# Kernel tuning notes

Measured on AMD Instinct MI355X. Metric: run time of the kernel, lower is better.

The kernel has to match this reference:

```python
import jax, jax.numpy as jnp
import numpy as np

N_NODES = {'movie': 50000, 'director': 10000, 'actor': 25000}
# relation name -> (src_type, dst_type, num_edges)
RELS = {'md': ('movie', 'director', 150000),
        'dm': ('director', 'movie', 150000),
        'ma': ('movie', 'actor', 300000),
        'am': ('actor', 'movie', 300000)}
F_IN, HID, HEADS, OUT = 1024, 256, 8, 4
HD = HID // HEADS  # 32 per-head dim


def setup_inputs() -> dict:
    key = jax.random.key(0)
    kit = iter(jax.random.split(key, 128))
    def nrm(shape, s):
        return jax.random.normal(next(kit), shape, jnp.float32) * s
    inp = {}
    for t, n in N_NODES.items():
        inp['x_' + t] = nrm((n, F_IN), 1.0)
    for rn, (st, dt, e) in RELS.items():
        inp['e_' + rn + '_src'] = jax.random.randint(next(kit), (e,), 0, N_NODES[st], dtype=jnp.int32)
        inp['e_' + rn + '_dst'] = jax.random.randint(next(kit), (e,), 0, N_NODES[dt], dtype=jnp.int32)
        inp['a_' + rn] = nrm((HEADS, HD, HD), 0.05)   # per-relation attention matrix
        inp['m_' + rn] = nrm((HEADS, HD, HD), 0.05)   # per-relation message matrix
        inp['p_' + rn] = jnp.ones((HEADS,), jnp.float32)  # relation priority
    for t in N_NODES:
        inp['W_in_' + t] = nrm((F_IN, HID), 0.02)
        inp['b_in_' + t] = jnp.zeros((HID,), jnp.float32)
        for nm in ('k', 'q', 'v'):
            inp['W' + nm + '_' + t] = nrm((HID, HID), 0.05)
            inp['b' + nm + '_' + t] = jnp.zeros((HID,), jnp.float32)
        inp['Wa_' + t] = nrm((HID, HID), 0.05)
        inp['ba_' + t] = jnp.zeros((HID,), jnp.float32)
        inp['skip_' + t] = jnp.array(1.0, jnp.float32)
    inp['W_out'] = nrm((HID, OUT), 0.05)
    inp['b_out'] = jnp.zeros((OUT,), jnp.float32)
    return inp


def _forward(p):
    # per-node-type input projection (the HGT.lin_dict step)
    h = {t: p['x_' + t] @ p['W_in_' + t] + p['b_in_' + t] for t in N_NODES}
    # per-type K/Q/V projections, reshaped to [N, H, D]
    def proj(nm):
        return {t: (h[t] @ p['W' + nm + '_' + t] + p['b' + nm + '_' + t]).reshape(-1, HEADS, HD)
                for t in N_NODES}
    k, q, v = proj('k'), proj('q'), proj('v')
    scale = 1.0 / np.sqrt(HD)
    # per-edge-type: gather, relation-transform, score
    buf = {t: [] for t in N_NODES}
    for rn, (st, dt, _) in RELS.items():
        si, di = p['e_' + rn + '_src'], p['e_' + rn + '_dst']
        ke = jnp.einsum('ehd,hdf->ehf', k[st][si], p['a_' + rn])  # [E,H,D]
        ve = jnp.einsum('ehd,hdf->ehf', v[st][si], p['m_' + rn])  # [E,H,D]
        al = (q[dt][di] * ke).sum(-1) * (p['p_' + rn] * scale)    # [E,H]
        buf[dt].append((di, al, ve))
    # destination-grouped segment softmax + scatter aggregation
    out = {}
    for t, n in N_NODES.items():
        di = jnp.concatenate([b[0] for b in buf[t]])
        al = jnp.concatenate([b[1] for b in buf[t]])
        ve = jnp.concatenate([b[2] for b in buf[t]])
        amax = jax.ops.segment_max(al, di, num_segments=n)        # [N,H]
        amax = jnp.where(jnp.isfinite(amax), amax, 0.0)
        ex = jnp.exp(al - amax[di])
        den = jax.ops.segment_sum(ex, di, num_segments=n)[di]
        w = ex / jnp.where(den > 0, den, 1.0)                     # [E,H]
        agg = jax.ops.segment_sum(w[:, :, None] * ve, di, num_segments=n).reshape(n, HID)
        o = jax.nn.gelu(agg @ p['Wa_' + t] + p['ba_' + t])
        beta = jax.nn.sigmoid(p['skip_' + t])                     # gated skip connection
        out[t] = beta * o + (1.0 - beta) * h[t]
    # final classifier on movie nodes
    return out['movie'] @ p['W_out'] + p['b_out']


def reference(x_movie, x_director, x_actor, e_md_src, e_md_dst, a_md, m_md, p_md, e_dm_src, e_dm_dst, a_dm, m_dm, p_dm, e_ma_src, e_ma_dst, a_ma, m_ma, p_ma, e_am_src, e_am_dst, a_am, m_am, p_am, W_in_movie, b_in_movie, Wk_movie, bk_movie, Wq_movie, bq_movie, Wv_movie, bv_movie, Wa_movie, ba_movie, skip_movie, W_in_director, b_in_director, Wk_director, bk_director, Wq_director, bq_director, Wv_director, bv_director, Wa_director, ba_director, skip_director, W_in_actor, b_in_actor, Wk_actor, bk_actor, Wq_actor, bq_actor, Wv_actor, bv_actor, Wa_actor, ba_actor, skip_actor, W_out, b_out):
    p = dict(locals())
    return _forward(p)
```

## Files before the change

kernel.cpp:

```cpp
#include <hip/hip_runtime.h>
#include <math.h>

#define NM 50000
#define ND 10000
#define NA 25000
#define E_DM 150000
#define E_AM 300000
#define E_TOT (E_DM + E_AM)
#define HID 256
#define HEADS 8
#define HD 32
#define FIN 1024
#define SCALE 0.17677669529663687f

typedef __attribute__((ext_vector_type(8))) short short8;
typedef __attribute__((ext_vector_type(4))) float f32x4;

typedef __attribute__((address_space(1))) const unsigned char gas_u8;
typedef __attribute__((address_space(3))) unsigned char las_u8;

__device__ __forceinline__ void gload16(const void* g, void* l) {
    gas_u8* gp = (gas_u8*)(unsigned long long)(uintptr_t)g;
    las_u8* lp = (las_u8*)(unsigned int)(uintptr_t)l;
    __builtin_amdgcn_global_load_lds((const __attribute__((address_space(1))) void*)gp,
                                     (__attribute__((address_space(3))) void*)lp, 16, 0, 0);
}

__device__ __forceinline__ unsigned int pk_bf16(float x, float y) {
    unsigned int a = __float_as_uint(x), b = __float_as_uint(y);
    a += 0x7FFFu + ((a >> 16) & 1u);
    b += 0x7FFFu + ((b >> 16) & 1u);
    return (a >> 16) | (b & 0xFFFF0000u);
}
__device__ __forceinline__ unsigned short to_bf16(float x) {
    unsigned int a = __float_as_uint(x);
    a += 0x7FFFu + ((a >> 16) & 1u);
    return (unsigned short)(a >> 16);
}
__device__ __forceinline__ float bf2f(unsigned short u) {
    return __uint_as_float(((unsigned int)u) << 16);
}

struct F4 { const float* W[4]; const float* b[4]; const float* a[4]; float* Wf[4]; float* bf[4]; };
__global__ void fold_w4(F4 f4) {
    int di = blockIdx.y;
    const float* W = f4.W[di]; const float* b = f4.b[di]; const float* a = f4.a[di];
    float* Wf = f4.Wf[di]; float* bf = f4.bf[di];
    int c = threadIdx.x;
    int h = c >> 5, f = c & 31;
    int r = blockIdx.x;
    float acc = 0.f;
    if (r < HID) {
        #pragma unroll
        for (int d = 0; d < HD; ++d)
            acc += W[r * HID + h * HD + d] * a[(h * HD + d) * HD + f];
        Wf[r * HID + c] = acc;
    } else {
        #pragma unroll
        for (int d = 0; d < HD; ++d)
            acc += b[h * HD + d] * a[(h * HD + d) * HD + f];
        bf[c] = acc;
    }
}

struct PDesc { const float* W; unsigned short* out; int K; int b0; };
struct PMulti { PDesc d[9]; int nd; };
__global__ void wt_pack(PMulti pm) {
    int bid = blockIdx.x; int di = 0;
    #pragma unroll
    for (int i = 1; i < 9; ++i) if (i < pm.nd && bid >= pm.d[i].b0) di = i;
    PDesc p = pm.d[di];
    int kstep = bid - p.b0;
    int t = threadIdx.x;
    #pragma unroll
    for (int i = 0; i < 32; ++i) {
        int idx = i * 256 + t;
        int n0 = idx >> 9, r = idx & 511, lane = r >> 3, j = r & 7;
        int k = kstep * 32 + (lane >> 4) * 8 + j;
        int c = n0 * 16 + (lane & 15);
        p.out[(size_t)kstep * 8192 + idx] = to_bf16(p.W[(size_t)k * HID + c]);
    }
}

struct GDesc {
    const void* A; const unsigned short* Bt; const float* bias; void* C;
    const void* hskip; const float* gate; int M; int K; int epi; int obf; int abf; int b0;
};
struct GMulti { GDesc d[5]; int nd; };

#define GBM 64

__launch_bounds__(512, 6)
__global__ void gemm_mfma(GMulti mu) {
    __shared__ unsigned short sB[2][16 * 512];
    __shared__ unsigned short sA[2][4 * 512];

    int bid = blockIdx.x;
    int di = 0;
    #pragma unroll
    for (int i = 1; i < 5; ++i)
        if (i < mu.nd && bid >= mu.d[i].b0) di = i;
    GDesc g = mu.d[di];
    int bm = (bid - g.b0) * GBM;
    int M = g.M, K = g.K;

    int t = threadIdx.x;
    int lane = t & 63;
    int w = t >> 6;
    int wp = w >> 1;
    int ch = w & 1;
    int l16 = lane & 15;

    int slot = t >> 1;
    int ss_ = slot >> 6;
    int sl  = slot & 63;
    int arow_f = bm + ss_ * 16 + (sl & 15);
    int ak0    = (sl >> 4) * 8 + (t & 1) * 4;
    const float* Ap = nullptr;
    const unsigned short* Abp = nullptr;
    if (g.abf) {
        if (w < 4) {
            int r = bm + w * 16 + l16;
            Abp = (const unsigned short*)g.A + (size_t)min(r, M - 1) * K + ((lane >> 4) * 8);
        }
    } else {
        Ap = (const float*)g.A + (size_t)min(arow_f, M - 1) * K + ak0;
    }

    f32x4 acc[8];
    #pragma unroll
    for (int n = 0; n < 8; ++n) acc[n] = (f32x4)(0.f);

    int nk = K >> 5;
    {
        const unsigned short* gB = g.Bt;
        gload16(gB + w * 512 + lane * 8, &sB[0][w * 512]);
        gload16(gB + (w + 8) * 512 + lane * 8, &sB[0][(w + 8) * 512]);
        if (g.abf) {
            if (w < 4) gload16(Abp, &sA[0][w * 512]);
        } else {
            float4 f = *(const float4*)(Ap);
            uint2 pk = make_uint2(pk_bf16(f.x, f.y), pk_bf16(f.z, f.w));
            *(uint2*)&sA[0][slot * 8 + (t & 1) * 4] = pk;
        }
    }
    __syncthreads();

    int cur = 0;
    for (int ks = 0; ks < nk; ++ks) {
        int nxt = cur ^ 1;
        bool pf = (ks + 1 < nk);
        float4 f;
        if (pf) {
            const unsigned short* gB = g.Bt + (size_t)(ks + 1) * 8192;
            gload16(gB + w * 512 + lane * 8, &sB[nxt][w * 512]);
            gload16(gB + (w + 8) * 512 + lane * 8, &sB[nxt][(w + 8) * 512]);
            if (g.abf) {
                if (w < 4) gload16(Abp + (ks + 1) * 32, &sA[nxt][w * 512]);
            } else {
                f = *(const float4*)(Ap + (ks + 1) * 32);
            }
        }
        short8 af = *(const short8*)&sA[cur][(wp * 64 + lane) * 8];
        short8 bfr[8];
        #pragma unroll
        for (int n = 0; n < 8; ++n)
            bfr[n] = *(const short8*)&sB[cur][((ch * 8 + n) * 64 + lane) * 8];
        #pragma unroll
        for (int n = 0; n < 8; ++n)
            acc[n] = __builtin_amdgcn_mfma_f32_16x16x32_bf16(af, bfr[n], acc[n], 0, 0, 0);
        if (pf && !g.abf) {
            uint2 pk = make_uint2(pk_bf16(f.x, f.y), pk_bf16(f.z, f.w));
            *(uint2*)&sA[nxt][slot * 8 + (t & 1) * 4] = pk;
        }
        __syncthreads();
        cur = nxt;
    }

    float beta = 0.f;
    if (g.epi) beta = 1.f / (1.f + expf(-g.gate[0]));
    int r0 = bm + wp * 16 + ((lane >> 4) << 2);
    #pragma unroll
    for (int n = 0; n < 8; ++n) {
        int col = ch * 128 + n * 16 + l16;
        #pragma unroll
        for (int j = 0; j < 4; ++j) {
            int grow = r0 + j;
            if (grow >= M) continue;
            float v = acc[n][j] + g.bias[col];
            if (g.epi) {
                float x = v;
                float gl = 0.5f * x * (1.f + tanhf(0.7978845608028654f * (x + 0.044715f * x * x * x)));
                float hv = bf2f(((const unsigned short*)g.hskip)[(size_t)grow * HID + col]);
                v = beta * gl + (1.f - beta) * hv;
            }
            if (g.obf) ((unsigned short*)g.C)[(size_t)grow * HID + col] = to_bf16(v);
            else ((float*)g.C)[(size_t)grow * HID + col] = v;
        }
    }
}

__global__ void hist_deg(const int* __restrict__ dA, const int* __restrict__ dB,
                         int* __restrict__ deg) {
    int i = blockIdx.x * 256 + threadIdx.x;
    if (i < E_DM) atomicAdd(&deg[dA[i]], 1);
    else if (i < E_TOT) atomicAdd(&deg[dB[i - E_DM]], 1);
}

__global__ void scan_pass1(const int* __restrict__ deg, int* __restrict__ bsum) {
    __shared__ int s[256];
    int b = blockIdx.x, t = threadIdx.x;
    int i = b * 256 + t;
    int v = (i < NM) ? deg[i] : 0;
    s[t] = v; __syncthreads();
    for (int off = 128; off > 0; off >>= 1) {
        if (t < off) s[t] += s[t + off];
        __syncthreads();
    }
    if (t == 0) bsum[b] = s[0];
}

__global__ void scan_pass2(const int* __restrict__ bsum, int* __restrict__ boff, int nb) {
    __shared__ int s[256];
    int t = threadIdx.x;
    int v = (t < nb) ? bsum[t] : 0;
    s[t] = v; __syncthreads();
    for (int off = 1; off < 256; off <<= 1) {
        int x = (t >= off) ? s[t - off] : 0;
        __syncthreads();
        s[t] += x;
        __syncthreads();
    }
    if (t < nb) boff[t] = s[t] - v;
}

__global__ void scan_pass3(const int* __restrict__ deg, const int* __restrict__ boff,
                           int* __restrict__ rowptr, int* __restrict__ cursor) {
    __shared__ int s[256];
    int b = blockIdx.x, t = threadIdx.x, i = b * 256 + t;
    int v = (i < NM) ? deg[i] : 0;
    s[t] = v; __syncthreads();
    for (int off = 1; off < 256; off <<= 1) {
        int x = (t >= off) ? s[t - off] : 0;
        __syncthreads();
        s[t] += x;
        __syncthreads();
    }
    int excl = s[t] - v + boff[b];
    if (i < NM) { rowptr[i] = excl; cursor[i] = excl; }
    if (i == 0) rowptr[NM] = E_TOT;
}

__global__ void fill_adj(const int* __restrict__ sA, const int* __restrict__ dA,
                         const int* __restrict__ sB, const int* __restrict__ dB,
                         int* __restrict__ cursor, int* __restrict__ adj) {
    int i = blockIdx.x * 256 + threadIdx.x;
    int d, entry;
    if (i < E_DM)      { d = dA[i];        entry = sA[i]; }
    else if (i < E_TOT){ int j = i - E_DM; d = dB[j]; entry = (sB[j] + ND) | (1 << 16); }
    else return;
    int pos = atomicAdd(&cursor[d], 1);
    adj[pos] = entry;
}

__launch_bounds__(256)
__global__ void agg_fused(const int* __restrict__ rowptr, const int* __restrict__ adj,
                          const unsigned short* __restrict__ q, const unsigned short* __restrict__ kt_all,
                          const unsigned short* __restrict__ vt_all,
                          const float* __restrict__ p_dm, const float* __restrict__ p_am,
                          unsigned short* __restrict__ agg) {
    int d = blockIdx.x * 4 + (threadIdx.x >> 6);
    if (d >= NM) return;
    int lane = threadIdx.x & 63;
    int h = lane >> 3;
    int start = rowptr[d], end = rowptr[d + 1];
    uint2 qu = *(const uint2*)(q + (size_t)d * HID + lane * 4);
    float q0 = __uint_as_float(qu.x << 16), q1 = __uint_as_float(qu.x & 0xFFFF0000u);
    float q2 = __uint_as_float(qu.y << 16), q3 = __uint_as_float(qu.y & 0xFFFF0000u);
    float pr0 = p_dm[h] * SCALE, pr1 = p_am[h] * SCALE;
    float m = -INFINITY, den = 0.f, a0 = 0.f, a1 = 0.f, a2 = 0.f, a3 = 0.f;
    for (int i = start; i < end; ++i) {
        int e = adj[i];
        int sr = e & 0xFFFF;
        uint2 ku = *(const uint2*)(kt_all + (size_t)sr * HID + lane * 4);
        float k0 = __uint_as_float(ku.x << 16), k1 = __uint_as_float(ku.x & 0xFFFF0000u);
        float k2 = __uint_as_float(ku.y << 16), k3 = __uint_as_float(ku.y & 0xFFFF0000u);
        float prod = q0 * k0 + q1 * k1 + q2 * k2 + q3 * k3;
        prod += __shfl_xor(prod, 1);
        prod += __shfl_xor(prod, 2);
        prod += __shfl_xor(prod, 4);
        float a = prod * ((e >> 16) ? pr1 : pr0);
        float mn = fmaxf(m, a);
        float c  = __expf(m - mn);
        float ex = __expf(a - mn);
        uint2 vu = *(const uint2*)(vt_all + (size_t)sr * HID + lane * 4);
        float v0 = __uint_as_float(vu.x << 16), v1 = __uint_as_float(vu.x & 0xFFFF0000u);
        float v2 = __uint_as_float(vu.y << 16), v3 = __uint_as_float(vu.y & 0xFFFF0000u);
        den = den * c + ex;
        a0 = a0 * c + ex * v0; a1 = a1 * c + ex * v1;
        a2 = a2 * c + ex * v2; a3 = a3 * c + ex * v3;
        m = mn;
    }
    float inv = (end > start) ? 1.f / den : 0.f;
    *(uint2*)(agg + (size_t)d * HID + lane * 4) =
        make_uint2(pk_bf16(a0 * inv, a1 * inv), pk_bf16(a2 * inv, a3 * inv));
}

__launch_bounds__(256)
__global__ void classifier(const float* __restrict__ X, const float* __restrict__ W,
                           const float* __restrict__ b, float* __restrict__ out, int M) {
    int t = threadIdx.x, lane = t & 63;
    int wid = blockIdx.x * 4 + (t >> 6);
    int nw = gridDim.x * 4;
    float w0[4], w1[4], w2[4], w3[4];
    #pragma unroll
    for (int j = 0; j < 4; ++j) {
        float4 wv = *(const float4*)(W + (lane * 4 + j) * 4);
        w0[j] = wv.x; w1[j] = wv.y; w2[j] = wv.z; w3[j] = wv.w;
    }
    float b0 = b[0], b1 = b[1], b2 = b[2], b3 = b[3];
    for (int row = wid; row < M; row += nw) {
        float4 x = *(const float4*)(X + (size_t)row * HID + lane * 4);
        float s0 = x.x * w0[0] + x.y * w0[1] + x.z * w0[2] + x.w * w0[3];
        float s1 = x.x * w1[0] + x.y * w1[1] + x.z * w1[2] + x.w * w1[3];
        float s2 = x.x * w2[0] + x.y * w2[1] + x.z * w2[2] + x.w * w2[3];
        float s3 = x.x * w3[0] + x.y * w3[1] + x.z * w3[2] + x.w * w3[3];
        #pragma unroll
        for (int off = 32; off > 0; off >>= 1) {
            s0 += __shfl_xor(s0, off); s1 += __shfl_xor(s1, off);
            s2 += __shfl_xor(s2, off); s3 += __shfl_xor(s3, off);
        }
        if (lane == 0) {
            float4 o = make_float4(s0 + b0, s1 + b1, s2 + b2, s3 + b3);
            *(float4*)(out + (size_t)row * 4) = o;
        }
    }
}

extern "C" void kernel_launch(void* const* d_in, const int* in_sizes, int n_in,
                              void* d_out, int out_size, void* d_ws, size_t ws_size,
                              hipStream_t stream) {
    (void)in_sizes; (void)n_in; (void)out_size; (void)ws_size;
    const float* x_movie    = (const float*)d_in[0];
    const float* x_director = (const float*)d_in[1];
    const float* x_actor    = (const float*)d_in[2];
    const int*   e_dm_src = (const int*)d_in[8];
    const int*   e_dm_dst = (const int*)d_in[9];
    const float* a_dm     = (const float*)d_in[10];
    const float* m_dm     = (const float*)d_in[11];
    const float* p_dm     = (const float*)d_in[12];
    const int*   e_am_src = (const int*)d_in[18];
    const int*   e_am_dst = (const int*)d_in[19];
    const float* a_am     = (const float*)d_in[20];
    const float* m_am     = (const float*)d_in[21];
    const float* p_am     = (const float*)d_in[22];
    const float* W_in_m = (const float*)d_in[23];
    const float* b_in_m = (const float*)d_in[24];
    const float* Wq_m   = (const float*)d_in[27];
    const float* bq_m   = (const float*)d_in[28];
    const float* Wa_m   = (const float*)d_in[31];
    const float* ba_m   = (const float*)d_in[32];
    const float* skip_m = (const float*)d_in[33];
    const float* W_in_d = (const float*)d_in[34];
    const float* b_in_d = (const float*)d_in[35];
    const float* Wk_d   = (const float*)d_in[36];
    const float* bk_d   = (const float*)d_in[37];
    const float* Wv_d   = (const float*)d_in[40];
    const float* bv_d   = (const float*)d_in[41];
    const float* W_in_a = (const float*)d_in[45];
    const float* b_in_a = (const float*)d_in[46];
    const float* Wk_a   = (const float*)d_in[47];
    const float* bk_a   = (const float*)d_in[48];
    const float* Wv_a   = (const float*)d_in[51];
    const float* bv_a   = (const float*)d_in[52];
    const float* W_out  = (const float*)d_in[56];
    const float* b_out  = (const float*)d_in[57];

    char* base = (char*)d_ws;
    size_t off = 0;
    auto alloc = [&](size_t bytes) -> void* {
        void* p = base + off;
        off = (off + bytes + 255) & ~(size_t)255;
        return p;
    };
    unsigned short* h_m = (unsigned short*)alloc((size_t)NM * HID * 2);
    unsigned short* h_d = (unsigned short*)alloc((size_t)ND * HID * 2);
    unsigned short* h_a = (unsigned short*)alloc((size_t)NA * HID * 2);
    unsigned short* q_m = (unsigned short*)alloc((size_t)NM * HID * 2);
    float* out_m  = (float*)alloc((size_t)NM * HID * 4);
    unsigned short* agg = (unsigned short*)alloc((size_t)NM * HID * 2);
    unsigned short* kt_all = (unsigned short*)alloc((size_t)(ND + NA) * HID * 2);
    unsigned short* vt_all = (unsigned short*)alloc((size_t)(ND + NA) * HID * 2);
    float* Wf     = (float*)alloc(4 * (size_t)HID * HID * 4);
    float* bf     = (float*)alloc(4 * (size_t)HID * 4);
    int* deg      = (int*)alloc(NM * 4);
    int* rowptr   = (int*)alloc((NM + 1) * 4);
    int* cursor   = (int*)alloc(NM * 4);
    int* bsum     = (int*)alloc(256 * 4);
    int* boff     = (int*)alloc(256 * 4);
    int* adj      = (int*)alloc((size_t)E_TOT * 4);
    unsigned short* Bt_in_m = (unsigned short*)alloc((size_t)256 * 1024 * 2);
    unsigned short* Bt_in_d = (unsigned short*)alloc((size_t)256 * 1024 * 2);
    unsigned short* Bt_in_a = (unsigned short*)alloc((size_t)256 * 1024 * 2);
    unsigned short* Bt_q_m  = (unsigned short*)alloc((size_t)256 * 256 * 2);
    unsigned short* Bt_k_dm = (unsigned short*)alloc((size_t)256 * 256 * 2);
    unsigned short* Bt_v_dm = (unsigned short*)alloc((size_t)256 * 256 * 2);
    unsigned short* Bt_k_am = (unsigned short*)alloc((size_t)256 * 256 * 2);
    unsigned short* Bt_v_am = (unsigned short*)alloc((size_t)256 * 256 * 2);
    unsigned short* Bt_a_m  = (unsigned short*)alloc((size_t)256 * 256 * 2);

    unsigned short* kt_dm = kt_all;
    unsigned short* kt_am = kt_all + (size_t)ND * HID;
    unsigned short* vt_dm = vt_all;
    unsigned short* vt_am = vt_all + (size_t)ND * HID;

    float* Wf_k_dm = Wf + 0 * HID * HID;  float* bf_k_dm = bf + 0 * HID;
    float* Wf_v_dm = Wf + 1 * HID * HID;  float* bf_v_dm = bf + 1 * HID;
    float* Wf_k_am = Wf + 2 * HID * HID;  float* bf_k_am = bf + 2 * HID;
    float* Wf_v_am = Wf + 3 * HID * HID;  float* bf_v_am = bf + 3 * HID;

    hipMemsetAsync(deg, 0, NM * sizeof(int), stream);
    hist_deg<<<(E_TOT + 255) / 256, 256, 0, stream>>>(e_dm_dst, e_am_dst, deg);
    int nb = (NM + 255) / 256;
    scan_pass1<<<nb, 256, 0, stream>>>(deg, bsum);
    scan_pass2<<<1, 256, 0, stream>>>(bsum, boff, nb);
    scan_pass3<<<nb, 256, 0, stream>>>(deg, boff, rowptr, cursor);
    fill_adj<<<(E_TOT + 255) / 256, 256, 0, stream>>>(e_dm_src, e_dm_dst, e_am_src, e_am_dst,
                                                      cursor, adj);

    {
        F4 f4{};
        f4.W[0] = Wk_d; f4.b[0] = bk_d; f4.a[0] = a_dm; f4.Wf[0] = Wf_k_dm; f4.bf[0] = bf_k_dm;
        f4.W[1] = Wv_d; f4.b[1] = bv_d; f4.a[1] = m_dm; f4.Wf[1] = Wf_v_dm; f4.bf[1] = bf_v_dm;
        f4.W[2] = Wk_a; f4.b[2] = bk_a; f4.a[2] = a_am; f4.Wf[2] = Wf_k_am; f4.bf[2] = bf_k_am;
        f4.W[3] = Wv_a; f4.b[3] = bv_a; f4.a[3] = m_am; f4.Wf[3] = Wf_v_am; f4.bf[3] = bf_v_am;
        fold_w4<<<dim3(257, 4), 256, 0, stream>>>(f4);
    }
    {
        PMulti pm{};
        pm.nd = 9;
        int b0 = 0;
        pm.d[0] = {W_in_m,  Bt_in_m, FIN, b0}; b0 += 32;
        pm.d[1] = {W_in_d,  Bt_in_d, FIN, b0}; b0 += 32;
        pm.d[2] = {W_in_a,  Bt_in_a, FIN, b0}; b0 += 32;
        pm.d[3] = {Wq_m,    Bt_q_m,  HID, b0}; b0 += 8;
        pm.d[4] = {Wf_k_dm, Bt_k_dm, HID, b0}; b0 += 8;
        pm.d[5] = {Wf_v_dm, Bt_v_dm, HID, b0}; b0 += 8;
        pm.d[6] = {Wf_k_am, Bt_k_am, HID, b0}; b0 += 8;
        pm.d[7] = {Wf_v_am, Bt_v_am, HID, b0}; b0 += 8;
        pm.d[8] = {Wa_m,    Bt_a_m,  HID, b0}; b0 += 8;
        wt_pack<<<b0, 256, 0, stream>>>(pm);
    }

    int bm_m = (NM + GBM - 1) / GBM;
    int bm_d = (ND + GBM - 1) / GBM;
    int bm_a = (NA + GBM - 1) / GBM;

    {
        GMulti mu{};
        mu.nd = 3;
        mu.d[0] = {x_movie,    Bt_in_m, b_in_m, h_m, nullptr, nullptr, NM, FIN, 0, 1, 0, 0};
        mu.d[1] = {x_director, Bt_in_d, b_in_d, h_d, nullptr, nullptr, ND, FIN, 0, 1, 0, bm_m};
        mu.d[2] = {x_actor,    Bt_in_a, b_in_a, h_a, nullptr, nullptr, NA, FIN, 0, 1, 0, bm_m + bm_d};
        gemm_mfma<<<bm_m + bm_d + bm_a, 512, 0, stream>>>(mu);
    }
    {
        GMulti mu{};
        mu.nd = 5;
        int b0 = 0;
        mu.d[0] = {h_m, Bt_q_m,  bq_m,    q_m,   nullptr, nullptr, NM, HID, 0, 1, 1, b0}; b0 += bm_m;
        mu.d[1] = {h_d, Bt_k_dm, bf_k_dm, kt_dm, nullptr, nullptr, ND, HID, 0, 1, 1, b0}; b0 += bm_d;
        mu.d[2] = {h_d, Bt_v_dm, bf_v_dm, vt_dm, nullptr, nullptr, ND, HID, 0, 1, 1, b0}; b0 += bm_d;
        mu.d[3] = {h_a, Bt_k_am, bf_k_am, kt_am, nullptr, nullptr, NA, HID, 0, 1, 1, b0}; b0 += bm_a;
        mu.d[4] = {h_a, Bt_v_am, bf_v_am, vt_am, nullptr, nullptr, NA, HID, 0, 1, 1, b0}; b0 += bm_a;
        gemm_mfma<<<b0, 512, 0, stream>>>(mu);
    }

    agg_fused<<<(NM + 3) / 4, 256, 0, stream>>>(rowptr, adj, q_m, kt_all, vt_all, p_dm, p_am, agg);

    {
        GMulti mu{};
        mu.nd = 1;
        mu.d[0] = {agg, Bt_a_m, ba_m, out_m, h_m, skip_m, NM, HID, 1, 0, 1, 0};
        gemm_mfma<<<bm_m, 512, 0, stream>>>(mu);
    }

    classifier<<<256, 256, 0, stream>>>(out_m, W_out, b_out, (float*)d_out, NM);
}
```

Before: 411.9 us.

## Fuse K/Q/V projections into input GEMM and classifier into output GEMM

The input-projection GEMM now stages its bf16 output tile in shared memory and immediately runs the second-stage Q or K/V projections from it, so director and actor hidden states never go to global memory and one GEMM launch disappears. The final attention-output GEMM folds the 256x4 classifier into its epilogue with shuffle and shared-memory reductions, which removes the fp32 out_m buffer and the separate classifier kernel. In exchange, the second-stage B operands are read straight from global memory without shared-memory staging, and the fused blocks do more serial work, which may lower the overlap available to the scheduler.

Result: faster. 361.2 us (median of 2 runs) (-12.3%).

```diff
diff --git a/kernel.cpp b/kernel.cpp
--- a/kernel.cpp
+++ b/kernel.cpp
@@ -84,7 +84,10 @@
 
 struct GDesc {
     const void* A; const unsigned short* Bt; const float* bias; void* C;
-    const void* hskip; const float* gate; int M; int K; int epi; int obf; int abf; int b0;
+    const void* hskip; const float* gate;
+    const unsigned short* Bt2; const float* bias2; void* C2;
+    const unsigned short* Bt3; const float* bias3; void* C3;
+    int M; int K; int epi; int obf; int abf; int cls; int b0;
 };
 struct GMulti { GDesc d[5]; int nd; };
 
@@ -92,8 +95,13 @@
 
 __launch_bounds__(512, 6)
 __global__ void gemm_mfma(GMulti mu) {
-    __shared__ unsigned short sB[2][16 * 512];
-    __shared__ unsigned short sA[2][4 * 512];
+    __shared__ __align__(16) unsigned char smem[40960];
+    unsigned short* sB0 = (unsigned short*)smem;
+    unsigned short* sB1 = sB0 + 8192;
+    unsigned short* sA0 = (unsigned short*)(smem + 32768);
+    unsigned short* sA1 = sA0 + 2048;
+    unsigned short* sHf = (unsigned short*)smem;
+    float* arr = (float*)smem;
 
     int bid = blockIdx.x;
     int di = 0;
@@ -134,68 +142,150 @@
     int nk = K >> 5;
     {
         const unsigned short* gB = g.Bt;
-        gload16(gB + w * 512 + lane * 8, &sB[0][w * 512]);
-        gload16(gB + (w + 8) * 512 + lane * 8, &sB[0][(w + 8) * 512]);
+        gload16(gB + w * 512 + lane * 8, sB0 + w * 512);
+        gload16(gB + (w + 8) * 512 + lane * 8, sB0 + (w + 8) * 512);
         if (g.abf) {
-            if (w < 4) gload16(Abp, &sA[0][w * 512]);
+            if (w < 4) gload16(Abp, sA0 + w * 512);
         } else {
             float4 f = *(const float4*)(Ap);
             uint2 pk = make_uint2(pk_bf16(f.x, f.y), pk_bf16(f.z, f.w));
-            *(uint2*)&sA[0][slot * 8 + (t & 1) * 4] = pk;
+            *(uint2*)&sA0[slot * 8 + (t & 1) * 4] = pk;
         }
     }
     __syncthreads();
 
     int cur = 0;
     for (int ks = 0; ks < nk; ++ks) {
-        int nxt = cur ^ 1;
+        unsigned short* sBc = cur ? sB1 : sB0;
+        unsigned short* sAc = cur ? sA1 : sA0;
+        unsigned short* dB  = cur ? sB0 : sB1;
+        unsigned short* dA  = cur ? sA0 : sA1;
         bool pf = (ks + 1 < nk);
         float4 f;
         if (pf) {
             const unsigned short* gB = g.Bt + (size_t)(ks + 1) * 8192;
-            gload16(gB + w * 512 + lane * 8, &sB[nxt][w * 512]);
-            gload16(gB + (w + 8) * 512 + lane * 8, &sB[nxt][(w + 8) * 512]);
+            gload16(gB + w * 512 + lane * 8, dB + w * 512);
+            gload16(gB + (w + 8) * 512 + lane * 8, dB + (w + 8) * 512);
             if (g.abf) {
-                if (w < 4) gload16(Abp + (ks + 1) * 32, &sA[nxt][w * 512]);
+                if (w < 4) gload16(Abp + (ks + 1) * 32, dA + w * 512);
             } else {
                 f = *(const float4*)(Ap + (ks + 1) * 32);
             }
         }
-        short8 af = *(const short8*)&sA[cur][(wp * 64 + lane) * 8];
+        short8 af = *(const short8*)&sAc[(wp * 64 + lane) * 8];
         short8 bfr[8];
         #pragma unroll
         for (int n = 0; n < 8; ++n)
-            bfr[n] = *(const short8*)&sB[cur][((ch * 8 + n) * 64 + lane) * 8];
+            bfr[n] = *(const short8*)&sBc[((ch * 8 + n) * 64 + lane) * 8];
         #pragma unroll
         for (int n = 0; n < 8; ++n)
             acc[n] = __builtin_amdgcn_mfma_f32_16x16x32_bf16(af, bfr[n], acc[n], 0, 0, 0);
         if (pf && !g.abf) {
             uint2 pk = make_uint2(pk_bf16(f.x, f.y), pk_bf16(f.z, f.w));
-            *(uint2*)&sA[nxt][slot * 8 + (t & 1) * 4] = pk;
-        }
-        __syncthreads();
-        cur = nxt;
+            *(uint2*)&dA[slot * 8 + (t & 1) * 4] = pk;
+        }
+        __syncthreads();
+        cur ^= 1;
     }
 
     float beta = 0.f;
     if (g.epi) beta = 1.f / (1.f + expf(-g.gate[0]));
     int r0 = bm + wp * 16 + ((lane >> 4) << 2);
+
+    float pcl[4][4];
+    if (g.cls) {
+        #pragma unroll
+        for (int j = 0; j < 4; ++j)
+            #pragma unroll
+            for (int c = 0; c < 4; ++c) pcl[j][c] = 0.f;
+    }
+
     #pragma unroll
     for (int n = 0; n < 8; ++n) {
         int col = ch * 128 + n * 16 + l16;
+        float4 wv;
+        if (g.cls) wv = *(const float4*)(g.bias2 + col * 4);
         #pragma unroll
         for (int j = 0; j < 4; ++j) {
             int grow = r0 + j;
-            if (grow >= M) continue;
             float v = acc[n][j] + g.bias[col];
             if (g.epi) {
                 float x = v;
                 float gl = 0.5f * x * (1.f + tanhf(0.7978845608028654f * (x + 0.044715f * x * x * x)));
-                float hv = bf2f(((const unsigned short*)g.hskip)[(size_t)grow * HID + col]);
+                float hv = bf2f(((const unsigned short*)g.hskip)[(size_t)min(grow, M - 1) * HID + col]);
                 v = beta * gl + (1.f - beta) * hv;
             }
-            if (g.obf) ((unsigned short*)g.C)[(size_t)grow * HID + col] = to_bf16(v);
-            else ((float*)g.C)[(size_t)grow * HID + col] = v;
+            if (g.cls) {
+                pcl[j][0] += v * wv.x; pcl[j][1] += v * wv.y;
+                pcl[j][2] += v * wv.z; pcl[j][3] += v * wv.w;
+            } else {
+                int ks2 = ch * 4 + (n >> 1);
+                int gg = ((n & 1) << 1) | ((lane & 15) >> 3);
+                int l = ((lane >> 4) << 2) + j + (gg << 4);
+                sHf[(((ks2 * 4) + wp) * 64 + l) * 8 + (lane & 7)] = to_bf16(v);
+                if (g.C && grow < M)
+                    ((unsigned short*)g.C)[(size_t)grow * HID + col] = to_bf16(v);
+            }
+        }
+    }
+
+    if (g.cls) {
+        #pragma unroll
+        for (int s = 1; s < 16; s <<= 1) {
+            #pragma unroll
+            for (int j = 0; j < 4; ++j)
+                #pragma unroll
+                for (int c = 0; c < 4; ++c)
+                    pcl[j][c] += __shfl_xor(pcl[j][c], s);
+        }
+        if (l16 == 0) {
+            int rb = wp * 16 + ((lane >> 4) << 2);
+            #pragma unroll
+            for (int j = 0; j < 4; ++j)
+                #pragma unroll
+                for (int c = 0; c < 4; ++c)
+                    arr[((ch * 64) + rb + j) * 4 + c] = pcl[j][c];
+        }
+        __syncthreads();
+        if (t < 256) {
+            int row = t >> 2, c = t & 3;
+            int grow = bm + row;
+            if (grow < M) {
+                float s = arr[(0 * 64 + row) * 4 + c] + arr[(1 * 64 + row) * 4 + c] + g.bias3[c];
+                ((float*)g.C2)[(size_t)grow * 4 + c] = s;
+            }
+        }
+    } else if (g.Bt2) {
+        __syncthreads();
+        #pragma unroll 1
+        for (int o = 0; o < 2; ++o) {
+            const unsigned short* B2 = o ? g.Bt3 : g.Bt2;
+            if (!B2) break;
+            const float* bias2 = o ? g.bias3 : g.bias2;
+            unsigned short* C2 = (unsigned short*)(o ? g.C3 : g.C2);
+            f32x4 acc2[8];
+            #pragma unroll
+            for (int n = 0; n < 8; ++n) acc2[n] = (f32x4)(0.f);
+            #pragma unroll 1
+            for (int ks = 0; ks < 8; ++ks) {
+                short8 af2 = *(const short8*)&sHf[(((ks * 4) + wp) * 64 + lane) * 8];
+                #pragma unroll
+                for (int n = 0; n < 8; ++n) {
+                    short8 b2 = *(const short8*)(B2 + (size_t)ks * 8192 +
+                                                 (size_t)(((ch * 8) + n) * 64 + lane) * 8);
+                    acc2[n] = __builtin_amdgcn_mfma_f32_16x16x32_bf16(af2, b2, acc2[n], 0, 0, 0);
+                }
+            }
+            #pragma unroll
+            for (int n = 0; n < 8; ++n) {
+                int col = ch * 128 + n * 16 + l16;
+                #pragma unroll
+                for (int j = 0; j < 4; ++j) {
+                    int grow = r0 + j;
+                    if (grow < M)
+                        C2[(size_t)grow * HID + col] = to_bf16(acc2[n][j] + bias2[col]);
+                }
+            }
         }
     }
 }
@@ -304,37 +394,6 @@
     float inv = (end > start) ? 1.f / den : 0.f;
     *(uint2*)(agg + (size_t)d * HID + lane * 4) =
         make_uint2(pk_bf16(a0 * inv, a1 * inv), pk_bf16(a2 * inv, a3 * inv));
-}
-
-__launch_bounds__(256)
-__global__ void classifier(const float* __restrict__ X, const float* __restrict__ W,
-                           const float* __restrict__ b, float* __restrict__ out, int M) {
-    int t = threadIdx.x, lane = t & 63;
-    int wid = blockIdx.x * 4 + (t >> 6);
-    int nw = gridDim.x * 4;
-    float w0[4], w1[4], w2[4], w3[4];
-    #pragma unroll
-    for (int j = 0; j < 4; ++j) {
-        float4 wv = *(const float4*)(W + (lane * 4 + j) * 4);
-        w0[j] = wv.x; w1[j] = wv.y; w2[j] = wv.z; w3[j] = wv.w;
-    }
-    float b0 = b[0], b1 = b[1], b2 = b[2], b3 = b[3];
-    for (int row = wid; row < M; row += nw) {
-        float4 x = *(const float4*)(X + (size_t)row * HID + lane * 4);
-        float s0 = x.x * w0[0] + x.y * w0[1] + x.z * w0[2] + x.w * w0[3];
-        float s1 = x.x * w1[0] + x.y * w1[1] + x.z * w1[2] + x.w * w1[3];
-        float s2 = x.x * w2[0] + x.y * w2[1] + x.z * w2[2] + x.w * w2[3];
-        float s3 = x.x * w3[0] + x.y * w3[1] + x.z * w3[2] + x.w * w3[3];
-        #pragma unroll
-        for (int off = 32; off > 0; off >>= 1) {
-            s0 += __shfl_xor(s0, off); s1 += __shfl_xor(s1, off);
-            s2 += __shfl_xor(s2, off); s3 += __shfl_xor(s3, off);
-        }
-        if (lane == 0) {
-            float4 o = make_float4(s0 + b0, s1 + b1, s2 + b2, s3 + b3);
-            *(float4*)(out + (size_t)row * 4) = o;
-        }
-    }
 }
 
 extern "C" void kernel_launch(void* const* d_in, const int* in_sizes, int n_in,
@@ -384,10 +443,7 @@
         return p;
     };
     unsigned short* h_m = (unsigned short*)alloc((size_t)NM * HID * 2);
-    unsigned short* h_d = (unsigned short*)alloc((size_t)ND * HID * 2);
-    unsigned short* h_a = (unsigned short*)alloc((size_t)NA * HID * 2);
     unsigned short* q_m = (unsigned short*)alloc((size_t)NM * HID * 2);
-    float* out_m  = (float*)alloc((size_t)NM * HID * 4);
     unsigned short* agg = (unsigned short*)alloc((size_t)NM * HID * 2);
     unsigned short* kt_all = (unsigned short*)alloc((size_t)(ND + NA) * HID * 2);
     unsigned short* vt_all = (unsigned short*)alloc((size_t)(ND + NA) * HID * 2);
@@ -459,21 +515,16 @@
     {
         GMulti mu{};
         mu.nd = 3;
-        mu.d[0] = {x_movie,    Bt_in_m, b_in_m, h_m, nullptr, nullptr, NM, FIN, 0, 1, 0, 0};
-        mu.d[1] = {x_director, Bt_in_d, b_in_d, h_d, nullptr, nullptr, ND, FIN, 0, 1, 0, bm_m};
-        mu.d[2] = {x_actor,    Bt_in_a, b_in_a, h_a, nullptr, nullptr, NA, FIN, 0, 1, 0, bm_m + bm_d};
+        mu.d[0] = {x_movie, Bt_in_m, b_in_m, h_m, nullptr, nullptr,
+                   Bt_q_m, bq_m, q_m, nullptr, nullptr, nullptr,
+                   NM, FIN, 0, 1, 0, 0, 0};
+        mu.d[1] = {x_director, Bt_in_d, b_in_d, nullptr, nullptr, nullptr,
+                   Bt_k_dm, bf_k_dm, kt_dm, Bt_v_dm, bf_v_dm, vt_dm,
+                   ND, FIN, 0, 1, 0, 0, bm_m};
+        mu.d[2] = {x_actor, Bt_in_a, b_in_a, nullptr, nullptr, nullptr,
+                   Bt_k_am, bf_k_am, kt_am, Bt_v_am, bf_v_am, vt_am,
+                   NA, FIN, 0, 1, 0, 0, bm_m + bm_d};
         gemm_mfma<<<bm_m + bm_d + bm_a, 512, 0, stream>>>(mu);
-    }
-    {
-        GMulti mu{};
-        mu.nd = 5;
-        int b0 = 0;
-        mu.d[0] = {h_m, Bt_q_m,  bq_m,    q_m,   nullptr, nullptr, NM, HID, 0, 1, 1, b0}; b0 += bm_m;
-        mu.d[1] = {h_d, Bt_k_dm, bf_k_dm, kt_dm, nullptr, nullptr, ND, HID, 0, 1, 1, b0}; b0 += bm_d;
-        mu.d[2] = {h_d, Bt_v_dm, bf_v_dm, vt_dm, nullptr, nullptr, ND, HID, 0, 1, 1, b0}; b0 += bm_d;
-        mu.d[3] = {h_a, Bt_k_am, bf_k_am, kt_am, nullptr, nullptr, NA, HID, 0, 1, 1, b0}; b0 += bm_a;
-        mu.d[4] = {h_a, Bt_v_am, bf_v_am, vt_am, nullptr, nullptr, NA, HID, 0, 1, 1, b0}; b0 += bm_a;
-        gemm_mfma<<<b0, 512, 0, stream>>>(mu);
     }
 
     agg_fused<<<(NM + 3) / 4, 256, 0, stream>>>(rowptr, adj, q_m, kt_all, vt_all, p_dm, p_am, agg);
@@ -481,9 +532,9 @@
     {
         GMulti mu{};
         mu.nd = 1;
-        mu.d[0] = {agg, Bt_a_m, ba_m, out_m, h_m, skip_m, NM, HID, 1, 0, 1, 0};
+        mu.d[0] = {agg, Bt_a_m, ba_m, nullptr, h_m, skip_m,
+                   nullptr, W_out, d_out, nullptr, b_out, nullptr,
+                   NM, HID, 1, 0, 1, 1, 0};
         gemm_mfma<<<bm_m, 512, 0, stream>>>(mu);
     }
-
-    classifier<<<256, 256, 0, stream>>>(out_m, W_out, b_out, (float*)d_out, NM);
-}
+}
```
